# Kernel optimization log

Hardware: AMD Instinct MI355X
Metric: run time of the kernel (lower is better)

The kernel has to match this reference:

```python
import jax, jax.numpy as jnp
import numpy as np

N, D = 262144, 512
EPS = 1e-6  # flax LayerNorm default


def setup_inputs() -> dict:
    key = jax.random.key(0)
    kx, kw = jax.random.split(key)
    x = jax.random.normal(kx, (N, D), dtype=jnp.float32)
    # LayerNorm params (flax defaults: scale init ones, bias init zeros)
    ln_scale = jnp.ones((D,), dtype=jnp.float32)
    ln_bias = jnp.zeros((D,), dtype=jnp.float32)
    # Dense params (lecun_normal kernel init approximated by scaled normal)
    kernel = jax.random.normal(kw, (D, D), dtype=jnp.float32) / jnp.sqrt(jnp.float32(D))
    bias = jnp.zeros((D,), dtype=jnp.float32)
    return {"x": x, "ln_scale": ln_scale, "ln_bias": ln_bias, "kernel": kernel, "bias": bias}


def reference(x, ln_scale, ln_bias, kernel, bias):
    # LayerNorm over last axis
    mu = jnp.mean(x, axis=-1, keepdims=True)
    var = jnp.mean(jnp.square(x - mu), axis=-1, keepdims=True)
    out = (x - mu) * jax.lax.rsqrt(var + EPS) * ln_scale + ln_bias
    # activation -> Dense -> residual add
    h = jax.nn.relu(out)
    return x + jnp.dot(h, kernel) + bias
```

## Files before the change

### kernel.cpp

```cpp
#include <hip/hip_runtime.h>
#include <hip/hip_bf16.h>

#define DD 512
#define BM 32
#define THREADS 512

typedef __attribute__((ext_vector_type(8))) short short8;
typedef __attribute__((ext_vector_type(4))) float f32x4;

__device__ __forceinline__ unsigned short f2bf(float f) {
  union { float f; unsigned u; } v; v.f = f;
  unsigned r = v.u + 0x7FFFu + ((v.u >> 16) & 1u);
  return (unsigned short)(r >> 16);
}
__device__ __forceinline__ float bf2f(unsigned short u) {
  union { unsigned u; float f; } v; v.u = ((unsigned)u) << 16;
  return v.f;
}

__global__ void prep_bpack(const float* __restrict__ W, unsigned short* __restrict__ Bpack) {
  const int tid = blockIdx.x * blockDim.x + threadIdx.x;
  const int n = tid & 511, k = tid >> 9;
  const float w = W[(size_t)k * DD + n];
  const int nb = n >> 4, lo = n & 15;
  const int kt = k >> 5, hi = (k >> 3) & 3, j = k & 7;
  const int lane = hi * 16 + lo;
  Bpack[(((size_t)(nb * 16 + kt)) * 64 + lane) * 8 + j] = f2bf(w);
}

__global__ __launch_bounds__(THREADS, 4)
void fused_ln_gemm(const float* __restrict__ x, const float* __restrict__ lns,
                   const float* __restrict__ lnb, const unsigned short* __restrict__ Bpack,
                   const float* __restrict__ bias, float* __restrict__ out) {
  __shared__ unsigned short Alds[BM * 512];
  __shared__ unsigned short Xlds[BM * 528];

  const int t = threadIdx.x;
  const long row0 = (long)blockIdx.x * BM;

  {
    const int r = t >> 4, g = t & 15;
    const float* xr = x + (row0 + r) * DD + g * 4;
    float4 v[8];
    float s = 0.f, s2 = 0.f;
    #pragma unroll
    for (int i = 0; i < 8; ++i) {
      v[i] = *(const float4*)(xr + i * 64);
      s  += (v[i].x + v[i].y) + (v[i].z + v[i].w);
      s2 += v[i].x * v[i].x + v[i].y * v[i].y + v[i].z * v[i].z + v[i].w * v[i].w;
    }
    #pragma unroll
    for (int m = 1; m < 16; m <<= 1) {
      s  += __shfl_xor(s,  m, 64);
      s2 += __shfl_xor(s2, m, 64);
    }
    const float mu   = s * (1.f / 512.f);
    const float var  = fmaxf(s2 * (1.f / 512.f) - mu * mu, 0.f);
    const float rstd = rsqrtf(var + 1e-6f);
    #pragma unroll
    for (int i = 0; i < 8; ++i) {
      const int c = g * 4 + i * 64;
      const float4 sc = *(const float4*)(lns + c);
      const float4 bi = *(const float4*)(lnb + c);
      float h0 = fmaxf((v[i].x - mu) * rstd * sc.x + bi.x, 0.f);
      float h1 = fmaxf((v[i].y - mu) * rstd * sc.y + bi.y, 0.f);
      float h2 = fmaxf((v[i].z - mu) * rstd * sc.z + bi.z, 0.f);
      float h3 = fmaxf((v[i].w - mu) * rstd * sc.w + bi.w, 0.f);
      ushort4 hu = { f2bf(h0), f2bf(h1), f2bf(h2), f2bf(h3) };
      ushort4 xu = { f2bf(v[i].x), f2bf(v[i].y), f2bf(v[i].z), f2bf(v[i].w) };
      unsigned a = (unsigned)(r * 1024 + g * 8 + i * 128) ^ (unsigned)((r & 7) << 4);
      *(ushort4*)((char*)Alds + a) = hu;
      *(ushort4*)(&Xlds[r * 528 + c]) = xu;
    }
  }
  __syncthreads();

  const int lane = t & 63, lo = lane & 15, hi = lane >> 4;
  const int wn = t >> 6;

  unsigned abase0, aswz0, abase1, aswz1;
  {
    const int r0 = lo;        abase0 = (unsigned)(r0 * 1024 + hi * 16); aswz0 = (unsigned)((r0 & 7) << 4);
    const int r1 = 16 + lo;   abase1 = (unsigned)(r1 * 1024 + hi * 16); aswz1 = (unsigned)((r1 & 7) << 4);
  }
  const short8* bbase = (const short8*)Bpack + (size_t)wn * 4096 + lane;

  short8 rb[3][4];
#define LOADB(s, kt)                                                          \
  { rb[s][0] = bbase[(0 * 16 + (kt)) * 64];                                   \
    rb[s][1] = bbase[(1 * 16 + (kt)) * 64];                                   \
    rb[s][2] = bbase[(2 * 16 + (kt)) * 64];                                   \
    rb[s][3] = bbase[(3 * 16 + (kt)) * 64]; }

  LOADB(0, 0);
  LOADB(1, 1);
  __builtin_amdgcn_sched_barrier(0);

  f32x4 acc00 = {}, acc01 = {}, acc02 = {}, acc03 = {};
  f32x4 acc10 = {}, acc11 = {}, acc12 = {}, acc13 = {};

  #pragma unroll
  for (int kt = 0; kt < 16; ++kt) {
    const int cur = kt % 3;
    if (kt + 2 < 16) {
      const int nxt = (kt + 2) % 3;
      LOADB(nxt, kt + 2);
    }
    __builtin_amdgcn_sched_barrier(0);
    const short8 a0 = *(const short8*)((const char*)Alds + ((abase0 + (unsigned)kt * 64) ^ aswz0));
    const short8 a1 = *(const short8*)((const char*)Alds + ((abase1 + (unsigned)kt * 64) ^ aswz1));
    acc00 = __builtin_amdgcn_mfma_f32_16x16x32_bf16(a0, rb[cur][0], acc00, 0, 0, 0);
    acc10 = __builtin_amdgcn_mfma_f32_16x16x32_bf16(a1, rb[cur][0], acc10, 0, 0, 0);
    acc01 = __builtin_amdgcn_mfma_f32_16x16x32_bf16(a0, rb[cur][1], acc01, 0, 0, 0);
    acc11 = __builtin_amdgcn_mfma_f32_16x16x32_bf16(a1, rb[cur][1], acc11, 0, 0, 0);
    acc02 = __builtin_amdgcn_mfma_f32_16x16x32_bf16(a0, rb[cur][2], acc02, 0, 0, 0);
    acc12 = __builtin_amdgcn_mfma_f32_16x16x32_bf16(a1, rb[cur][2], acc12, 0, 0, 0);
    acc03 = __builtin_amdgcn_mfma_f32_16x16x32_bf16(a0, rb[cur][3], acc03, 0, 0, 0);
    acc13 = __builtin_amdgcn_mfma_f32_16x16x32_bf16(a1, rb[cur][3], acc13, 0, 0, 0);
  }
#undef LOADB

  f32x4 accs[2][4] = {{acc00, acc01, acc02, acc03}, {acc10, acc11, acc12, acc13}};
  #pragma unroll
  for (int m = 0; m < 2; ++m) {
    #pragma unroll
    for (int nt = 0; nt < 4; ++nt) {
      const int col = wn * 64 + nt * 16 + lo;
      const float bv = bias[col];
      #pragma unroll
      for (int q = 0; q < 4; ++q) {
        const int rloc = m * 16 + hi * 4 + q;
        const float xv = bf2f(Xlds[rloc * 528 + col]);
        out[(row0 + rloc) * DD + col] = xv + accs[m][nt][q] + bv;
      }
    }
  }
}

extern "C" void kernel_launch(void* const* d_in, const int* in_sizes, int n_in,
                              void* d_out, int out_size, void* d_ws, size_t ws_size,
                              hipStream_t stream) {
  const float* x    = (const float*)d_in[0];
  const float* lns  = (const float*)d_in[1];
  const float* lnb  = (const float*)d_in[2];
  const float* W    = (const float*)d_in[3];
  const float* bias = (const float*)d_in[4];
  float* out = (float*)d_out;
  unsigned short* Bpack = (unsigned short*)d_ws;

  const int nrows = in_sizes[0] / DD;

  prep_bpack<<<DD * DD / 256, 256, 0, stream>>>(W, Bpack);
  fused_ln_gemm<<<nrows / BM, THREADS, 0, stream>>>(x, lns, lnb, Bpack, bias, out);
}
```

Baseline: 314.0 us.

## Double row tile to 64 with 1024 threads and 4x2 MFMA warp tiling

Raises the block's row tile from 32 to 64 rows and the thread count from 512 to 1024. Each of the 16 waves now covers all 64 rows and a 32-column slice (4x2 MFMA tiles) instead of 32 rows by 64 columns, so the packed weight is read from L2 half as often per output row. The residual-x copy in LDS now uses the same XOR swizzle as the activation tile instead of a padded stride. Risks: LDS use grows to about 128KB per block, so only one block fits per CU, and the launch bound of 4 blocks at 1024 threads may squeeze the register allocation.

```diff
diff --git a/kernel.cpp b/kernel.cpp
--- a/kernel.cpp
+++ b/kernel.cpp
@@ -2,8 +2,8 @@
 #include <hip/hip_bf16.h>
 
 #define DD 512
-#define BM 32
-#define THREADS 512
+#define BM 64
+#define THREADS 1024
 
 typedef __attribute__((ext_vector_type(8))) short short8;
 typedef __attribute__((ext_vector_type(4))) float f32x4;
@@ -33,9 +33,11 @@
                    const float* __restrict__ lnb, const unsigned short* __restrict__ Bpack,
                    const float* __restrict__ bias, float* __restrict__ out) {
   __shared__ unsigned short Alds[BM * 512];
-  __shared__ unsigned short Xlds[BM * 528];
+  __shared__ unsigned short Xlds[BM * 512];
 
   const int t = threadIdx.x;
+  const int lane = t & 63, lo = lane & 15, hi = lane >> 4;
+  const int w = t >> 6;
   const long row0 = (long)blockIdx.x * BM;
 
   {
@@ -62,42 +64,37 @@
       const int c = g * 4 + i * 64;
       const float4 sc = *(const float4*)(lns + c);
       const float4 bi = *(const float4*)(lnb + c);
-      float h0 = fmaxf((v[i].x - mu) * rstd * sc.x + bi.x, 0.f);
-      float h1 = fmaxf((v[i].y - mu) * rstd * sc.y + bi.y, 0.f);
-      float h2 = fmaxf((v[i].z - mu) * rstd * sc.z + bi.z, 0.f);
-      float h3 = fmaxf((v[i].w - mu) * rstd * sc.w + bi.w, 0.f);
-      ushort4 hu = { f2bf(h0), f2bf(h1), f2bf(h2), f2bf(h3) };
+      ushort4 hu;
+      hu.x = f2bf(fmaxf((v[i].x - mu) * rstd * sc.x + bi.x, 0.f));
+      hu.y = f2bf(fmaxf((v[i].y - mu) * rstd * sc.y + bi.y, 0.f));
+      hu.z = f2bf(fmaxf((v[i].z - mu) * rstd * sc.z + bi.z, 0.f));
+      hu.w = f2bf(fmaxf((v[i].w - mu) * rstd * sc.w + bi.w, 0.f));
       ushort4 xu = { f2bf(v[i].x), f2bf(v[i].y), f2bf(v[i].z), f2bf(v[i].w) };
-      unsigned a = (unsigned)(r * 1024 + g * 8 + i * 128) ^ (unsigned)((r & 7) << 4);
+      const unsigned a = (unsigned)(r * 1024 + g * 8 + i * 128) ^ (unsigned)((r & 7) << 4);
       *(ushort4*)((char*)Alds + a) = hu;
-      *(ushort4*)(&Xlds[r * 528 + c]) = xu;
+      *(ushort4*)((char*)Xlds + a) = xu;
     }
   }
   __syncthreads();
 
-  const int lane = t & 63, lo = lane & 15, hi = lane >> 4;
-  const int wn = t >> 6;
+  unsigned abase[4];
+  #pragma unroll
+  for (int m = 0; m < 4; ++m)
+    abase[m] = (unsigned)((m * 16 + lo) * 1024 + hi * 16);
+  const unsigned asw = (unsigned)((lo & 7) << 4);
 
-  unsigned abase0, aswz0, abase1, aswz1;
-  {
-    const int r0 = lo;        abase0 = (unsigned)(r0 * 1024 + hi * 16); aswz0 = (unsigned)((r0 & 7) << 4);
-    const int r1 = 16 + lo;   abase1 = (unsigned)(r1 * 1024 + hi * 16); aswz1 = (unsigned)((r1 & 7) << 4);
-  }
-  const short8* bbase = (const short8*)Bpack + (size_t)wn * 4096 + lane;
+  const short8* bbase = (const short8*)Bpack + (size_t)(w * 2) * 1024 + lane;
 
-  short8 rb[3][4];
+  short8 rb[3][2];
 #define LOADB(s, kt)                                                          \
   { rb[s][0] = bbase[(0 * 16 + (kt)) * 64];                                   \
-    rb[s][1] = bbase[(1 * 16 + (kt)) * 64];                                   \
-    rb[s][2] = bbase[(2 * 16 + (kt)) * 64];                                   \
-    rb[s][3] = bbase[(3 * 16 + (kt)) * 64]; }
+    rb[s][1] = bbase[(1 * 16 + (kt)) * 64]; }
 
   LOADB(0, 0);
   LOADB(1, 1);
   __builtin_amdgcn_sched_barrier(0);
 
-  f32x4 acc00 = {}, acc01 = {}, acc02 = {}, acc03 = {};
-  f32x4 acc10 = {}, acc11 = {}, acc12 = {}, acc13 = {};
+  f32x4 acc[4][2] = {};
 
   #pragma unroll
   for (int kt = 0; kt < 16; ++kt) {
@@ -107,32 +104,32 @@
       LOADB(nxt, kt + 2);
     }
     __builtin_amdgcn_sched_barrier(0);
-    const short8 a0 = *(const short8*)((const char*)Alds + ((abase0 + (unsigned)kt * 64) ^ aswz0));
-    const short8 a1 = *(const short8*)((const char*)Alds + ((abase1 + (unsigned)kt * 64) ^ aswz1));
-    acc00 = __builtin_amdgcn_mfma_f32_16x16x32_bf16(a0, rb[cur][0], acc00, 0, 0, 0);
-    acc10 = __builtin_amdgcn_mfma_f32_16x16x32_bf16(a1, rb[cur][0], acc10, 0, 0, 0);
-    acc01 = __builtin_amdgcn_mfma_f32_16x16x32_bf16(a0, rb[cur][1], acc01, 0, 0, 0);
-    acc11 = __builtin_amdgcn_mfma_f32_16x16x32_bf16(a1, rb[cur][1], acc11, 0, 0, 0);
-    acc02 = __builtin_amdgcn_mfma_f32_16x16x32_bf16(a0, rb[cur][2], acc02, 0, 0, 0);
-    acc12 = __builtin_amdgcn_mfma_f32_16x16x32_bf16(a1, rb[cur][2], acc12, 0, 0, 0);
-    acc03 = __builtin_amdgcn_mfma_f32_16x16x32_bf16(a0, rb[cur][3], acc03, 0, 0, 0);
-    acc13 = __builtin_amdgcn_mfma_f32_16x16x32_bf16(a1, rb[cur][3], acc13, 0, 0, 0);
+    short8 a[4];
+    #pragma unroll
+    for (int m = 0; m < 4; ++m)
+      a[m] = *(const short8*)((const char*)Alds + ((abase[m] + (unsigned)kt * 64) ^ asw));
+    #pragma unroll
+    for (int m = 0; m < 4; ++m) {
+      acc[m][0] = __builtin_amdgcn_mfma_f32_16x16x32_bf16(a[m], rb[cur][0], acc[m][0], 0, 0, 0);
+      acc[m][1] = __builtin_amdgcn_mfma_f32_16x16x32_bf16(a[m], rb[cur][1], acc[m][1], 0, 0, 0);
+    }
   }
 #undef LOADB
 
-  f32x4 accs[2][4] = {{acc00, acc01, acc02, acc03}, {acc10, acc11, acc12, acc13}};
+  const int col0 = w * 32 + lo;
+  const float bv0 = bias[col0];
+  const float bv1 = bias[col0 + 16];
   #pragma unroll
-  for (int m = 0; m < 2; ++m) {
+  for (int m = 0; m < 4; ++m) {
     #pragma unroll
-    for (int nt = 0; nt < 4; ++nt) {
-      const int col = wn * 64 + nt * 16 + lo;
-      const float bv = bias[col];
-      #pragma unroll
-      for (int q = 0; q < 4; ++q) {
-        const int rloc = m * 16 + hi * 4 + q;
-        const float xv = bf2f(Xlds[rloc * 528 + col]);
-        out[(row0 + rloc) * DD + col] = xv + accs[m][nt][q] + bv;
-      }
+    for (int q = 0; q < 4; ++q) {
+      const int rl = m * 16 + hi * 4 + q;
+      const unsigned xb = (unsigned)(rl * 1024 + col0 * 2) ^ (unsigned)((rl & 7) << 4);
+      const float xv0 = bf2f(*(const unsigned short*)((const char*)Xlds + xb));
+      const float xv1 = bf2f(*(const unsigned short*)((const char*)Xlds + (xb ^ 32u)));
+      float* o = out + (row0 + rl) * DD + col0;
+      o[0]  = acc[m][0][q] + xv0 + bv0;
+      o[16] = acc[m][1][q] + xv1 + bv1;
     }
   }
 }
```

After: 295.4 us. 1.06x faster.
